# Optimization experiments

Hardware: AMD Instinct MI355X
Metric: run time of the kernel (lower is better)

## Reference

```python
import jax, jax.numpy as jnp
import numpy as np

NUM_GROUPS = 32
EPS = 1e-5


def group_norm(x, scale, bias):
    # x: [B, C, L], normalize per (group, batch) over (C//G, L)
    B, C, L = x.shape
    G = NUM_GROUPS
    xg = x.reshape(B, G, C // G, L)
    mean = xg.mean(axis=(2, 3), keepdims=True)
    var = xg.var(axis=(2, 3), keepdims=True)
    xg = (xg - mean) * jax.lax.rsqrt(var + EPS)
    h = xg.reshape(B, C, L)
    return h * scale[None, :, None] + bias[None, :, None]


def setup_inputs() -> dict:
    key = jax.random.key(0)
    ks = jax.random.split(key, 8)
    B, C, L = 8, 512, 2048
    s = 1.0 / np.sqrt(C)
    return {
        "x": jax.random.normal(ks[0], (B, C, L), jnp.float32),
        "gn_scale": jnp.ones((C,), jnp.float32),
        "gn_bias": jnp.zeros((C,), jnp.float32),
        "wq": jax.random.normal(ks[1], (C, C), jnp.float32) * s,
        "bq": jnp.zeros((C,), jnp.float32),
        "wk": jax.random.normal(ks[2], (C, C), jnp.float32) * s,
        "bk": jnp.zeros((C,), jnp.float32),
        "wv": jax.random.normal(ks[3], (C, C), jnp.float32) * s,
        "bv": jnp.zeros((C,), jnp.float32),
        "wo": jax.random.normal(ks[4], (C, C), jnp.float32) * s,
        "bo": jnp.zeros((C,), jnp.float32),
    }


def reference(x, gn_scale, gn_bias, wq, bq, wk, bk, wv, bv, wo, bo):
    B, C, L = x.shape
    h = group_norm(x, gn_scale, gn_bias)  # [B, C, L]
    # 1x1 conv == per-position linear; produce [B, L, C] directly
    q = jnp.einsum('oc,bcl->blo', wq, h) + bq
    k = jnp.einsum('oc,bcl->blo', wk, h) + bk
    v = jnp.einsum('oc,bcl->blo', wv, h) + bv
    scale = jnp.asarray(C, x.dtype) ** -0.5
    w = jnp.einsum('bqc,bkc->bqk', q, k) * scale  # [B, L, L]
    w = jax.nn.softmax(w, axis=-1)
    a = jnp.einsum('bqk,bkc->bqc', w, v)  # [B, L, C]
    out = jnp.einsum('oc,blc->bol', wo, a) + bo[None, :, None]  # [B, C, L]
    return x + out
```

## Files before the change

### kernel.cpp

```cpp
#include <hip/hip_runtime.h>

typedef __attribute__((ext_vector_type(8))) _Float16 half8;
typedef __attribute__((ext_vector_type(4))) float floatx4;

#define AS1 __attribute__((address_space(1)))
#define AS3 __attribute__((address_space(3)))

__device__ __forceinline__ void async_load16(const void* g, void* l) {
  __builtin_amdgcn_global_load_lds((AS1 void*)(unsigned long long)g,
                                   (AS3 void*)(unsigned long long)l, 16, 0, 0);
}

template <int N>
__device__ __forceinline__ void wait_vm() {
  static_assert(N >= 0 && N <= 12, "extend wait_vm");
  if constexpr (N == 0) asm volatile("s_waitcnt vmcnt(0)" ::: "memory");
  else if constexpr (N == 1) asm volatile("s_waitcnt vmcnt(1)" ::: "memory");
  else if constexpr (N == 2) asm volatile("s_waitcnt vmcnt(2)" ::: "memory");
  else if constexpr (N == 3) asm volatile("s_waitcnt vmcnt(3)" ::: "memory");
  else if constexpr (N == 4) asm volatile("s_waitcnt vmcnt(4)" ::: "memory");
  else if constexpr (N == 5) asm volatile("s_waitcnt vmcnt(5)" ::: "memory");
  else if constexpr (N == 6) asm volatile("s_waitcnt vmcnt(6)" ::: "memory");
  else if constexpr (N == 7) asm volatile("s_waitcnt vmcnt(7)" ::: "memory");
  else if constexpr (N == 8) asm volatile("s_waitcnt vmcnt(8)" ::: "memory");
  else if constexpr (N == 9) asm volatile("s_waitcnt vmcnt(9)" ::: "memory");
  else if constexpr (N == 10) asm volatile("s_waitcnt vmcnt(10)" ::: "memory");
  else if constexpr (N == 11) asm volatile("s_waitcnt vmcnt(11)" ::: "memory");
  else asm volatile("s_waitcnt vmcnt(12)" ::: "memory");
}

__global__ __launch_bounds__(256) void gn_stats(const float* __restrict__ x,
                                                float* __restrict__ stats) {
  const int bg = blockIdx.x;
  const float4* p4 = (const float4*)(x + (long long)bg * 32768);
  const int t = threadIdx.x;
  float s = 0.f, ss = 0.f;
  for (int i = t; i < 8192; i += 256) {
    float4 v = p4[i];
    s += v.x + v.y + v.z + v.w;
    ss += v.x * v.x + v.y * v.y + v.z * v.z + v.w * v.w;
  }
#pragma unroll
  for (int off = 32; off; off >>= 1) { s += __shfl_down(s, off); ss += __shfl_down(ss, off); }
  __shared__ float rs[4], rss[4];
  if ((t & 63) == 0) { rs[t >> 6] = s; rss[t >> 6] = ss; }
  __syncthreads();
  if (t == 0) {
    s = rs[0] + rs[1] + rs[2] + rs[3];
    ss = rss[0] + rss[1] + rss[2] + rss[3];
    float mean = s * (1.f / 32768.f);
    float var = ss * (1.f / 32768.f) - mean * mean;
    stats[bg] = mean;
    stats[256 + bg] = rsqrtf(var + 1e-5f);
  }
}

__global__ __launch_bounds__(256) void gn_apply(const float* __restrict__ x,
                                                const float* __restrict__ stats,
                                                const float* __restrict__ gsc,
                                                const float* __restrict__ gbi,
                                                _Float16* __restrict__ ht) {
  __shared__ float tile[64][65];
  const int b = blockIdx.z, c0 = blockIdx.y * 64, l0 = blockIdx.x * 64;
  const int t = threadIdx.x, tr = t >> 6, tc = t & 63;
  const float* xb = x + ((long long)b * 512 + c0) * 2048 + l0;
#pragma unroll
  for (int p = 0; p < 16; ++p) {
    int row = tr + p * 4;
    tile[row][tc] = xb[(long long)row * 2048 + tc];
  }
  __syncthreads();
  const int c = c0 + tc;
  const int bg = b * 32 + (c >> 4);
  const float mean = stats[bg], rstd = stats[256 + bg];
  const float sc = gsc[c] * rstd;
  const float off = gbi[c] - mean * sc;
  _Float16* hb = ht + ((long long)b * 2048 + l0) * 512 + c0;
#pragma unroll
  for (int p = 0; p < 16; ++p) {
    int l = tr + p * 4;
    hb[(long long)l * 512 + tc] = (_Float16)(tile[tc][l] * sc + off);
  }
}

__global__ __launch_bounds__(256) void cast_w(const float* __restrict__ w0, const float* __restrict__ w1,
                                              const float* __restrict__ w2, const float* __restrict__ w3,
                                              const float* __restrict__ bq, const float* __restrict__ bk,
                                              _Float16* __restrict__ outw, float* __restrict__ bqk) {
  const long long i = (long long)blockIdx.x * 256 + threadIdx.x;
  if (blockIdx.x < 4096) {
    const int m = (int)(i >> 18);
    const int r = (int)(i & 262143);
    const float* w = (m == 0) ? w0 : (m == 1) ? w1 : (m == 2) ? w2 : w3;
    outw[i] = (_Float16)w[r];
  } else {
    const int j = (int)(i - 4096LL * 256);
    bqk[j] = (j < 512) ? bq[j] : bk[j - 512];
  }
}

template <int BM, int BN, int BIAS_MODE , int OUT_TYPE , bool RESIDUAL>
__global__ __launch_bounds__(512, 2) void gemm2p(
    const _Float16* __restrict__ A, long long sA, int lda,
    const _Float16* __restrict__ Bt, long long sB, int ldb,
    void* __restrict__ Cv, long long sC, int ldc,
    const float* __restrict__ bias,
    const float* __restrict__ resid, long long sR,
    float alpha, int K) {
  constexpr int ASZ = BM * 64, BSZ = BN * 64;
  constexpr int BUF = ASZ + BSZ;
  constexpr int RWA = BM / 16, RWB = BN / 16;
  constexpr int LA = RWA / 8, LB = RWB / 8;
  constexpr int L = 2 * LA + 2 * LB;
  constexpr int NMI = BM / 64, NNJ = BN / 128;
  __shared__ __align__(16) _Float16 ls[2 * BUF];

  const int tid = threadIdx.x;
  const int wave = tid >> 6, lane = tid & 63;
  const int wr = wave >> 2, wc = wave & 3;
  const int fm = lane & 15, q = lane >> 4;
  const int bz = blockIdx.x;
  const int m0 = blockIdx.y * BM, n0 = blockIdx.z * BN;
  A += (long long)bz * sA;
  Bt += (long long)bz * sB;

  const int srow = lane >> 3;
  const int schunk = ((lane & 7) ^ (srow & 7)) * 8;
  const _Float16* pA0 = A + (long long)(m0 + RWA * wave + srow) * lda + schunk;
  const _Float16* pA1 = pA0 + (long long)(BM / 2) * lda;
  const _Float16* pB0 = Bt + (long long)(n0 + RWB * wave + srow) * ldb + schunk;
  const _Float16* pB1 = pB0 + (long long)(BN / 2) * ldb;
  const int dA0 = RWA * wave * 64;
  const int dB0 = ASZ + RWB * wave * 64;

  const int c0 = (q ^ (fm & 7)) * 8;
  const int c1 = ((q + 4) ^ (fm & 7)) * 8;
  const int arow = wr * (BM / 4) + fm;
  const int brow = wc * (BN / 8) + fm;

  floatx4 acc[2][2][NMI][NNJ] = {};
  half8 af[NMI][2], bf0[NNJ][2], bf1[NNJ][2];

  const int NT = K >> 6;

  {
    _Float16* st = ls;
#pragma unroll
    for (int s = 0; s < LA; ++s) async_load16(pA0 + (long long)(8 * s) * lda, st + dA0 + s * 512);
#pragma unroll
    for (int s = 0; s < LB; ++s) async_load16(pB0 + (long long)(8 * s) * ldb, st + dB0 + s * 512);
#pragma unroll
    for (int s = 0; s < LB; ++s) async_load16(pB1 + (long long)(8 * s) * ldb, st + dB0 + BSZ / 2 + s * 512);
#pragma unroll
    for (int s = 0; s < LA; ++s) async_load16(pA1 + (long long)(8 * s) * lda, st + dA0 + ASZ / 2 + s * 512);
    pA0 += 64; pA1 += 64; pB0 += 64; pB1 += 64;
    wait_vm<0>();
  }

#define G8_READ_A(MH)                                                      \
  _Pragma("unroll") for (int mi = 0; mi < NMI; ++mi) {                     \
    const int r_ = (MH) * (BM / 2) + arow + 16 * mi;                       \
    af[mi][0] = *(const half8*)&cb[r_ * 64 + c0];                          \
    af[mi][1] = *(const half8*)&cb[r_ * 64 + c1];                          \
  }
#define G8_READ_B(NH, BF)                                                  \
  _Pragma("unroll") for (int nj = 0; nj < NNJ; ++nj) {                     \
    const int r_ = ASZ + ((NH) * (BN / 2) + brow + 16 * nj) * 64;          \
    BF[nj][0] = *(const half8*)&cb[r_ + c0];                               \
    BF[nj][1] = *(const half8*)&cb[r_ + c1];                               \
  }
#define G8_MFMA(MH, NH, BF)                                                \
  __builtin_amdgcn_s_setprio(1);                                           \
  _Pragma("unroll") for (int mi = 0; mi < NMI; ++mi)                       \
  _Pragma("unroll") for (int nj = 0; nj < NNJ; ++nj) {                     \
    acc[MH][NH][mi][nj] = __builtin_amdgcn_mfma_f32_16x16x32_f16(          \
        af[mi][0], BF[nj][0], acc[MH][NH][mi][nj], 0, 0, 0);               \
    acc[MH][NH][mi][nj] = __builtin_amdgcn_mfma_f32_16x16x32_f16(          \
        af[mi][1], BF[nj][1], acc[MH][NH][mi][nj], 0, 0, 0);               \
  }                                                                        \
  __builtin_amdgcn_s_setprio(0);
#define G8_STAGE_A(PTR, OFF)                                               \
  _Pragma("unroll") for (int s = 0; s < LA; ++s)                           \
    async_load16(PTR + (long long)(8 * s) * lda, st + dA0 + (OFF) + s * 512);
#define G8_STAGE_B(PTR, OFF)                                               \
  _Pragma("unroll") for (int s = 0; s < LB; ++s)                           \
    async_load16(PTR + (long long)(8 * s) * ldb, st + dB0 + (OFF) + s * 512);

  for (int kt = 0; kt < NT - 1; ++kt) {
    const _Float16* cb = ls + (kt & 1) * BUF;
    _Float16* st = ls + ((kt + 1) & 1) * BUF;
    __builtin_amdgcn_s_barrier();
    G8_READ_A(0)
    G8_READ_B(0, bf0)
    G8_READ_B(1, bf1)
    G8_STAGE_A(pA0, 0)
    G8_STAGE_B(pB0, 0)
    G8_STAGE_B(pB1, BSZ / 2)
    G8_STAGE_A(pA1, ASZ / 2)
    pA0 += 64; pA1 += 64; pB0 += 64; pB1 += 64;
    wait_vm<L>();
    G8_MFMA(0, 0, bf0)
    G8_MFMA(0, 1, bf1)
    __builtin_amdgcn_s_barrier();
    G8_READ_A(1)
    wait_vm<LA>();
    G8_MFMA(1, 1, bf1)
    G8_MFMA(1, 0, bf0)
  }
  {
    const _Float16* cb = ls + ((NT - 1) & 1) * BUF;
    __builtin_amdgcn_s_barrier();
    G8_READ_A(0)
    G8_READ_B(0, bf0)
    G8_READ_B(1, bf1)
    wait_vm<0>();
    G8_MFMA(0, 0, bf0)
    G8_MFMA(0, 1, bf1)
    __builtin_amdgcn_s_barrier();
    G8_READ_A(1)
    G8_MFMA(1, 1, bf1)
    G8_MFMA(1, 0, bf0)
  }

#undef G8_READ_A
#undef G8_READ_B
#undef G8_MFMA
#undef G8_STAGE_A
#undef G8_STAGE_B

#pragma unroll
  for (int mh = 0; mh < 2; ++mh)
#pragma unroll
    for (int nh = 0; nh < 2; ++nh)
#pragma unroll
      for (int mi = 0; mi < NMI; ++mi)
#pragma unroll
        for (int nj = 0; nj < NNJ; ++nj) {
          const int rr0 = m0 + mh * (BM / 2) + wr * (BM / 4) + 16 * mi + 4 * q;
          const int cc = n0 + nh * (BN / 2) + wc * (BN / 8) + 16 * nj + fm;
#pragma unroll
          for (int t = 0; t < 4; ++t) {
            const int rr = rr0 + t;
            float v = acc[mh][nh][mi][nj][t] * alpha;
            if (BIAS_MODE == 1) v += bias[cc];
            if (BIAS_MODE == 2) v += bias[rr];
            if (RESIDUAL) v += resid[(long long)bz * sR + (long long)rr * ldc + cc];
            const long long off = (long long)bz * sC + (long long)rr * ldc + cc;
            if (OUT_TYPE == 0) ((float*)Cv)[off] = v;
            else ((_Float16*)Cv)[off] = (_Float16)v;
          }
        }
}

__global__ __launch_bounds__(256) void softmax_inplace(_Float16* __restrict__ S) {
  const long long row = (long long)blockIdx.y * 2048 + blockIdx.x;
  _Float16* p = S + row * 2048;
  const int t = threadIdx.x;
  union U { float4 f; _Float16 h[8]; } u;
  u.f = ((const float4*)p)[t];
  float v[8];
  float mx = -3e38f;
#pragma unroll
  for (int i = 0; i < 8; ++i) { v[i] = (float)u.h[i]; mx = fmaxf(mx, v[i]); }
#pragma unroll
  for (int off = 32; off; off >>= 1) mx = fmaxf(mx, __shfl_down(mx, off));
  __shared__ float red[4];
  if ((t & 63) == 0) red[t >> 6] = mx;
  __syncthreads();
  mx = fmaxf(fmaxf(red[0], red[1]), fmaxf(red[2], red[3]));
  float s = 0.f;
#pragma unroll
  for (int i = 0; i < 8; ++i) { v[i] = __expf(v[i] - mx); s += v[i]; }
#pragma unroll
  for (int off = 32; off; off >>= 1) s += __shfl_down(s, off);
  __syncthreads();
  if ((t & 63) == 0) red[t >> 6] = s;
  __syncthreads();
  s = red[0] + red[1] + red[2] + red[3];
  const float inv = 1.f / s;
#pragma unroll
  for (int i = 0; i < 8; ++i) u.h[i] = (_Float16)(v[i] * inv);
  ((float4*)p)[t] = u.f;
}

extern "C" void kernel_launch(void* const* d_in, const int* in_sizes, int n_in,
                              void* d_out, int out_size, void* d_ws, size_t ws_size,
                              hipStream_t stream) {
  const float* x = (const float*)d_in[0];
  const float* gsc = (const float*)d_in[1];
  const float* gbi = (const float*)d_in[2];
  const float* wq = (const float*)d_in[3];
  const float* bq = (const float*)d_in[4];
  const float* wk = (const float*)d_in[5];
  const float* bk = (const float*)d_in[6];
  const float* wv = (const float*)d_in[7];
  const float* bv = (const float*)d_in[8];
  const float* wo = (const float*)d_in[9];
  const float* bo = (const float*)d_in[10];
  float* out = (float*)d_out;

  char* ws = (char*)d_ws;
  float* stats = (float*)ws;
  float* bqk = (float*)(ws + 2048);
  _Float16* wbf = (_Float16*)(ws + 8192);
  _Float16* ht = wbf + 4 * 262144;
  const long long EB = 8LL * 2048 * 512;
  _Float16* qk = ht + EB;
  _Float16* vm = qk + 2 * EB;
  _Float16* Sb = vm + EB;
  _Float16* at = ht;

  gn_stats<<<256, 256, 0, stream>>>(x, stats);
  gn_apply<<<dim3(32, 8, 8), 256, 0, stream>>>(x, stats, gsc, gbi, ht);
  cast_w<<<4100, 256, 0, stream>>>(wq, wk, wv, wo, bq, bk, wbf, bqk);

  const float scale = 0.044194173824159216f;
  gemm2p<256, 256, 1, 1, false><<<dim3(8, 8, 4), 512, 0, stream>>>(
      ht, 1048576LL, 512, wbf, 0LL, 512, qk, 2097152LL, 1024, bqk, nullptr, 0LL, 1.f, 512);
  gemm2p<128, 256, 2, 1, false><<<dim3(8, 4, 8), 512, 0, stream>>>(
      wbf + 2 * 262144, 0LL, 512, ht, 1048576LL, 512, vm, 1048576LL, 2048, bv, nullptr, 0LL, 1.f, 512);
  gemm2p<256, 256, 0, 1, false><<<dim3(8, 8, 8), 512, 0, stream>>>(
      qk, 2097152LL, 1024, qk + 512, 2097152LL, 1024, Sb, 4194304LL, 2048, nullptr, nullptr, 0LL, scale, 512);
  softmax_inplace<<<dim3(2048, 8), 256, 0, stream>>>(Sb);
  gemm2p<128, 256, 0, 1, false><<<dim3(8, 16, 2), 512, 0, stream>>>(
      Sb, 4194304LL, 2048, vm, 1048576LL, 2048, at, 1048576LL, 512, nullptr, nullptr, 0LL, 1.f, 2048);
  gemm2p<128, 256, 2, 0, true><<<dim3(8, 4, 8), 512, 0, stream>>>(
      wbf + 3 * 262144, 0LL, 512, at, 1048576LL, 512, out, 1048576LL, 2048, bo, x, 1048576LL, 1.f, 512);
}
```

Before: 289.6 us.

## Fuse softmax normalization into PV GEMM via precomputed row max/sum stats

Replaces the in-place softmax kernel with a row_stats kernel that only reads the scores and writes a per-row (max, 1/sum) pair. A new dedicated PV GEMM loads raw scores through registers, applies exp and normalization while staging them into LDS, and DMAs V asynchronously. This removes the full write-back of the normalized score matrix, at the cost of recomputing exp inside the GEMM and putting register-path loads on the A operand. The MFMA loop order in the generic GEMM is also changed to iterate the k-halves on the outside.

Measured after the change: 277.2 us. 4.3% less time.

```diff
diff --git a/kernel.cpp b/kernel.cpp
--- a/kernel.cpp
+++ b/kernel.cpp
@@ -171,13 +171,11 @@
   }
 #define G8_MFMA(MH, NH, BF)                                                \
   __builtin_amdgcn_s_setprio(1);                                           \
+  _Pragma("unroll") for (int kk = 0; kk < 2; ++kk)                         \
   _Pragma("unroll") for (int mi = 0; mi < NMI; ++mi)                       \
-  _Pragma("unroll") for (int nj = 0; nj < NNJ; ++nj) {                     \
+  _Pragma("unroll") for (int nj = 0; nj < NNJ; ++nj)                       \
     acc[MH][NH][mi][nj] = __builtin_amdgcn_mfma_f32_16x16x32_f16(          \
-        af[mi][0], BF[nj][0], acc[MH][NH][mi][nj], 0, 0, 0);               \
-    acc[MH][NH][mi][nj] = __builtin_amdgcn_mfma_f32_16x16x32_f16(          \
-        af[mi][1], BF[nj][1], acc[MH][NH][mi][nj], 0, 0, 0);               \
-  }                                                                        \
+        af[mi][kk], BF[nj][kk], acc[MH][NH][mi][nj], 0, 0, 0);             \
   __builtin_amdgcn_s_setprio(0);
 #define G8_STAGE_A(PTR, OFF)                                               \
   _Pragma("unroll") for (int s = 0; s < LA; ++s)                           \
@@ -252,9 +250,10 @@
         }
 }
 
-__global__ __launch_bounds__(256) void softmax_inplace(_Float16* __restrict__ S) {
+__global__ __launch_bounds__(256) void row_stats(const _Float16* __restrict__ S,
+                                                 float2* __restrict__ rms) {
   const long long row = (long long)blockIdx.y * 2048 + blockIdx.x;
-  _Float16* p = S + row * 2048;
+  const _Float16* p = S + row * 2048;
   const int t = threadIdx.x;
   union U { float4 f; _Float16 h[8]; } u;
   u.f = ((const float4*)p)[t];
@@ -270,17 +269,146 @@
   mx = fmaxf(fmaxf(red[0], red[1]), fmaxf(red[2], red[3]));
   float s = 0.f;
 #pragma unroll
-  for (int i = 0; i < 8; ++i) { v[i] = __expf(v[i] - mx); s += v[i]; }
+  for (int i = 0; i < 8; ++i) s += __expf(v[i] - mx);
 #pragma unroll
   for (int off = 32; off; off >>= 1) s += __shfl_down(s, off);
   __syncthreads();
   if ((t & 63) == 0) red[t >> 6] = s;
   __syncthreads();
-  s = red[0] + red[1] + red[2] + red[3];
-  const float inv = 1.f / s;
-#pragma unroll
-  for (int i = 0; i < 8; ++i) u.h[i] = (_Float16)(v[i] * inv);
-  ((float4*)p)[t] = u.f;
+  if (t == 0) {
+    s = red[0] + red[1] + red[2] + red[3];
+    rms[blockIdx.y * 2048 + blockIdx.x] = make_float2(mx, 1.f / s);
+  }
+}
+
+__global__ __launch_bounds__(512, 2) void gemm_pv(
+    const _Float16* __restrict__ S, const float2* __restrict__ rms,
+    const _Float16* __restrict__ Vt, _Float16* __restrict__ Out) {
+  constexpr int BM = 128, BN = 256;
+  constexpr int ASZ = BM * 64, BSZ = BN * 64, BUF = ASZ + BSZ;
+  constexpr int LB = 2;
+  constexpr int NMI = 2, NNJ = 2;
+  constexpr int NT = 32;
+  __shared__ __align__(16) _Float16 ls[2 * BUF];
+
+  const int tid = threadIdx.x;
+  const int wave = tid >> 6, lane = tid & 63;
+  const int wr = wave >> 2, wc = wave & 3;
+  const int fm = lane & 15, q = lane >> 4;
+  const int bz = blockIdx.x;
+  const int m0 = blockIdx.y * BM, n0 = blockIdx.z * BN;
+
+  const int srow = lane >> 3;
+  const int schunk = ((lane & 7) ^ (srow & 7)) * 8;
+  const int rA0 = m0 + 8 * wave + srow;
+  const float2 st0 = rms[bz * 2048 + rA0];
+  const float2 st1 = rms[bz * 2048 + rA0 + 64];
+  const _Float16* pA0 = S + (long long)bz * 4194304 + (long long)rA0 * 2048 + schunk;
+  const _Float16* pA1 = pA0 + 64LL * 2048;
+  const _Float16* pB0 = Vt + (long long)bz * 1048576 + (long long)(n0 + 16 * wave + srow) * 2048 + schunk;
+  const _Float16* pB1 = pB0 + 128LL * 2048;
+  const int dA0 = 8 * wave * 64;
+  const int dB0 = ASZ + 16 * wave * 64;
+
+  const int c0 = (q ^ (fm & 7)) * 8;
+  const int c1 = ((q + 4) ^ (fm & 7)) * 8;
+  const int arow = wr * (BM / 4) + fm;
+  const int brow = wc * (BN / 8) + fm;
+
+  floatx4 acc[2][2][NMI][NNJ] = {};
+  half8 afx[2][NMI][2], bfx[2][NNJ][2];
+
+#define PV_EXPW(DST, RA, MM, INV)                                          \
+  { half8 pe_;                                                             \
+    _Pragma("unroll") for (int e = 0; e < 8; ++e)                          \
+      pe_[e] = (_Float16)(__expf((float)(RA)[e] - (MM)) * (INV));          \
+    *(half8*)(DST) = pe_; }
+#define PV_DMA_B(PTR, OFF)                                                 \
+  _Pragma("unroll") for (int s = 0; s < LB; ++s)                           \
+    async_load16(PTR + (long long)(8 * s) * 2048, stb + dB0 + (OFF) + s * 512);
+
+  {
+    _Float16* stb = ls;
+    half8 ra0 = *(const half8*)pA0;
+    half8 ra1 = *(const half8*)pA1;
+    PV_DMA_B(pB0, 0)
+    PV_DMA_B(pB1, BSZ / 2)
+    PV_EXPW(&stb[dA0 + lane * 8], ra0, st0.x, st0.y)
+    PV_EXPW(&stb[dA0 + ASZ / 2 + lane * 8], ra1, st1.x, st1.y)
+    pA0 += 64; pA1 += 64; pB0 += 64; pB1 += 64;
+    asm volatile("s_waitcnt vmcnt(0) lgkmcnt(0)" ::: "memory");
+  }
+
+  for (int kt = 0; kt < NT; ++kt) {
+    const _Float16* cb = ls + (kt & 1) * BUF;
+    _Float16* stb = ls + ((kt + 1) & 1) * BUF;
+    __builtin_amdgcn_s_barrier();
+#pragma unroll
+    for (int mh = 0; mh < 2; ++mh)
+#pragma unroll
+      for (int mi = 0; mi < NMI; ++mi) {
+        const int r_ = mh * (BM / 2) + arow + 16 * mi;
+        afx[mh][mi][0] = *(const half8*)&cb[r_ * 64 + c0];
+        afx[mh][mi][1] = *(const half8*)&cb[r_ * 64 + c1];
+      }
+#pragma unroll
+    for (int nh = 0; nh < 2; ++nh)
+#pragma unroll
+      for (int nj = 0; nj < NNJ; ++nj) {
+        const int r_ = ASZ + (nh * (BN / 2) + brow + 16 * nj) * 64;
+        bfx[nh][nj][0] = *(const half8*)&cb[r_ + c0];
+        bfx[nh][nj][1] = *(const half8*)&cb[r_ + c1];
+      }
+    half8 ra0, ra1;
+    const bool more = (kt < NT - 1);
+    if (more) {
+      ra0 = *(const half8*)pA0;
+      ra1 = *(const half8*)pA1;
+      PV_DMA_B(pB0, 0)
+      PV_DMA_B(pB1, BSZ / 2)
+      pB0 += 64; pB1 += 64;
+    }
+    __builtin_amdgcn_s_setprio(1);
+#pragma unroll
+    for (int kk = 0; kk < 2; ++kk)
+#pragma unroll
+      for (int mh = 0; mh < 2; ++mh)
+#pragma unroll
+        for (int mi = 0; mi < NMI; ++mi)
+#pragma unroll
+          for (int nh = 0; nh < 2; ++nh)
+#pragma unroll
+            for (int nj = 0; nj < NNJ; ++nj)
+              acc[mh][nh][mi][nj] = __builtin_amdgcn_mfma_f32_16x16x32_f16(
+                  afx[mh][mi][kk], bfx[nh][nj][kk], acc[mh][nh][mi][nj], 0, 0, 0);
+    __builtin_amdgcn_s_setprio(0);
+    if (more) {
+      PV_EXPW(&stb[dA0 + lane * 8], ra0, st0.x, st0.y)
+      PV_EXPW(&stb[dA0 + ASZ / 2 + lane * 8], ra1, st1.x, st1.y)
+      pA0 += 64; pA1 += 64;
+    }
+    asm volatile("s_waitcnt vmcnt(0) lgkmcnt(0)" ::: "memory");
+  }
+#undef PV_EXPW
+#undef PV_DMA_B
+
+#pragma unroll
+  for (int mh = 0; mh < 2; ++mh)
+#pragma unroll
+    for (int nh = 0; nh < 2; ++nh)
+#pragma unroll
+      for (int mi = 0; mi < NMI; ++mi)
+#pragma unroll
+        for (int nj = 0; nj < NNJ; ++nj) {
+          const int rr0 = m0 + mh * (BM / 2) + wr * (BM / 4) + 16 * mi + 4 * q;
+          const int cc = n0 + nh * (BN / 2) + wc * (BN / 8) + 16 * nj + fm;
+#pragma unroll
+          for (int t = 0; t < 4; ++t) {
+            const int rr = rr0 + t;
+            Out[(long long)bz * 1048576 + (long long)rr * 512 + cc] =
+                (_Float16)acc[mh][nh][mi][nj][t];
+          }
+        }
 }
 
 extern "C" void kernel_launch(void* const* d_in, const int* in_sizes, int n_in,
@@ -309,6 +437,7 @@
   _Float16* vm = qk + 2 * EB;
   _Float16* Sb = vm + EB;
   _Float16* at = ht;
+  float2* rms = (float2*)qk;
 
   gn_stats<<<256, 256, 0, stream>>>(x, stats);
   gn_apply<<<dim3(32, 8, 8), 256, 0, stream>>>(x, stats, gsc, gbi, ht);
@@ -321,9 +450,8 @@
       wbf + 2 * 262144, 0LL, 512, ht, 1048576LL, 512, vm, 1048576LL, 2048, bv, nullptr, 0LL, 1.f, 512);
   gemm2p<256, 256, 0, 1, false><<<dim3(8, 8, 8), 512, 0, stream>>>(
       qk, 2097152LL, 1024, qk + 512, 2097152LL, 1024, Sb, 4194304LL, 2048, nullptr, nullptr, 0LL, scale, 512);
-  softmax_inplace<<<dim3(2048, 8), 256, 0, stream>>>(Sb);
-  gemm2p<128, 256, 0, 1, false><<<dim3(8, 16, 2), 512, 0, stream>>>(
-      Sb, 4194304LL, 2048, vm, 1048576LL, 2048, at, 1048576LL, 512, nullptr, nullptr, 0LL, 1.f, 2048);
+  row_stats<<<dim3(2048, 8), 256, 0, stream>>>(Sb, rms);
+  gemm_pv<<<dim3(8, 16, 2), 512, 0, stream>>>(Sb, rms, vm, at);
   gemm2p<128, 256, 2, 0, true><<<dim3(8, 4, 8), 512, 0, stream>>>(
       wbf + 3 * 262144, 0LL, 512, at, 1048576LL, 512, out, 1048576LL, 2048, bo, x, 1048576LL, 1.f, 512);
 }
```
